# Kernel optimization log

Hardware: AMD Instinct MI355X
Metric: run time of the kernel (lower is better)

The kernel has to match this reference:

```python
import jax, jax.numpy as jnp
import numpy as np

N_NODES = 50000
N_EDGES = 600000
N_COMM = 500
COMM_EDGES = 8000
NFEAT = 128
NHID = 128
NCLASS = 10
NLAYERS = 3
NHEADS = 8
EPS = 1e-5


def setup_inputs() -> dict:
    key = jax.random.key(0)
    ks = jax.random.split(key, 32)
    s = 0.05
    def rn(i, shape, scale=s):
        return (jax.random.normal(ks[i], shape, dtype=jnp.float32) * scale)
    return {
        "node_features": jax.random.normal(ks[0], (N_NODES, NFEAT), dtype=jnp.float32),
        "node_edge_index": jax.random.randint(ks[1], (2, N_EDGES), 0, N_NODES),
        "comm_features": jax.random.normal(ks[2], (N_COMM, NHID), dtype=jnp.float32),
        "comm_edge_index": jax.random.randint(ks[3], (2, COMM_EDGES), 0, N_COMM),
        "node_to_comm_map": jax.random.randint(ks[4], (N_NODES,), 0, N_COMM),
        # node-branch GCN params (nfeat == nhid so weights stack)
        "node_W": rn(5, (NLAYERS, NHID, NHID)),
        "node_b": rn(6, (NLAYERS, NHID)),
        "node_bn_g": 1.0 + rn(7, (NLAYERS, NHID)),
        "node_bn_b": rn(8, (NLAYERS, NHID)),
        # community-branch GCN params
        "comm_W": rn(9, (NLAYERS, NHID, NHID)),
        "comm_b": rn(10, (NLAYERS, NHID)),
        "comm_bn_g": 1.0 + rn(11, (NLAYERS, NHID)),
        "comm_bn_b": rn(12, (NLAYERS, NHID)),
        # MultiheadAttention params (torch layout: y = x @ W.T + b)
        "attn_in_w": rn(13, (3 * NHID, NHID)),
        "attn_in_b": rn(14, (3 * NHID,)),
        "attn_out_w": rn(15, (NHID, NHID)),
        "attn_out_b": rn(16, (NHID,)),
        # gate LayerNorm
        "ln_g": 1.0 + rn(17, (NHID,)),
        "ln_b": rn(18, (NHID,)),
        # classifier: Linear(128,64) -> BN -> ReLU -> Linear(64,10)
        "cls_W1": rn(19, (NHID, NHID // 2)),
        "cls_b1": rn(20, (NHID // 2,)),
        "cls_bn_g": 1.0 + rn(21, (NHID // 2,)),
        "cls_bn_b": rn(22, (NHID // 2,)),
        "cls_W2": rn(23, (NHID // 2, NCLASS)),
        "cls_b2": rn(24, (NCLASS,)),
    }


def _gcn_norm(edge_index, n):
    # PyG gcn_norm: add self-loops, symmetric D^-1/2 (A+I) D^-1/2
    loop = jnp.arange(n)
    src = jnp.concatenate([edge_index[0], loop])
    dst = jnp.concatenate([edge_index[1], loop])
    deg = jax.ops.segment_sum(jnp.ones(src.shape[0], jnp.float32), dst, num_segments=n)
    dinv = jnp.where(deg > 0, deg ** -0.5, 0.0)
    return src, dst, dinv[src] * dinv[dst]


def _gcn_stack(x, edge_index, Ws, bs, gs, betas):
    n = x.shape[0]
    src, dst, norm = _gcn_norm(edge_index, n)
    h = x
    for i in range(Ws.shape[0]):
        h_prev = h
        m = h @ Ws[i]  # linear commutes with normalized aggregation
        agg = jax.ops.segment_sum(m[src] * norm[:, None], dst, num_segments=n) + bs[i]
        mu = agg.mean(0)
        var = agg.var(0)  # biased, as torch BN training
        hb = (agg - mu) / jnp.sqrt(var + EPS) * gs[i] + betas[i]
        h = jax.nn.relu(hb)
        if i > 0:
            h = h + h_prev
    return h


def _mha(x, wi, bi, wo, bo):
    # x: [N, S=2, E]
    N, S, E = x.shape
    dh = E // NHEADS
    qkv = x @ wi.T + bi
    q, k, v = jnp.split(qkv, 3, axis=-1)
    q = q.reshape(N, S, NHEADS, dh)
    k = k.reshape(N, S, NHEADS, dh)
    v = v.reshape(N, S, NHEADS, dh)
    att = jnp.einsum('nqhd,nkhd->nhqk', q, k) / np.float32(np.sqrt(dh))
    att = jax.nn.softmax(att, axis=-1)
    o = jnp.einsum('nhqk,nkhd->nqhd', att, v).reshape(N, S, E)
    return o @ wo.T + bo


def reference(node_features, node_edge_index, comm_features, comm_edge_index,
              node_to_comm_map, node_W, node_b, node_bn_g, node_bn_b,
              comm_W, comm_b, comm_bn_g, comm_bn_b,
              attn_in_w, attn_in_b, attn_out_w, attn_out_b,
              ln_g, ln_b, cls_W1, cls_b1, cls_bn_g, cls_bn_b, cls_W2, cls_b2):
    h_node = _gcn_stack(node_features, node_edge_index, node_W, node_b, node_bn_g, node_bn_b)
    h_comm = _gcn_stack(comm_features, comm_edge_index, comm_W, comm_b, comm_bn_g, comm_bn_b)
    safe = jnp.clip(node_to_comm_map, 0, h_comm.shape[0] - 1)
    h_comm_exp = h_comm[safe]  # [N, nhid] cross-scale gather
    comb = jnp.stack([h_node, h_comm_exp], axis=1)  # [N, 2, nhid]
    attended = _mha(comb, attn_in_w, attn_in_b, attn_out_w, attn_out_b)
    x = attended.mean(axis=1) + h_node
    mu = x.mean(-1, keepdims=True)
    var = x.var(-1, keepdims=True)
    h_final = (x - mu) / jnp.sqrt(var + EPS) * ln_g + ln_b
    z = h_final @ cls_W1 + cls_b1
    zm = z.mean(0)
    zv = z.var(0)
    z = jax.nn.relu((z - zm) / jnp.sqrt(zv + EPS) * cls_bn_g + cls_bn_b)
    logits = z @ cls_W2 + cls_b2
    return jax.nn.log_softmax(logits, axis=-1)
```

## Files before the change

### kernel.cpp

```cpp
#include <hip/hip_runtime.h>
#include <hip/hip_bf16.h>
#include <cstdint>
#include <cstddef>


typedef __attribute__((ext_vector_type(8))) short bf16x8;
typedef __attribute__((ext_vector_type(4))) float f32x4;

#define EPSV 1e-5f

__device__ __forceinline__ float b2f(unsigned short u) {
    union { unsigned int i; float f; } x; x.i = ((unsigned int)u) << 16; return x.f;
}
__device__ __forceinline__ unsigned short f2b(float f) {
    union { float f; unsigned int i; } x; x.f = f;
    unsigned int i = x.i;
    return (unsigned short)((i + 0x7fffu + ((i >> 16) & 1u)) >> 16);
}

__global__ void prep_kernel(const float* __restrict__ node_W, const float* __restrict__ comm_W,
                            const float* __restrict__ cls_W1, const float* __restrict__ attn_in_w,
                            const float* __restrict__ attn_out_w, const float* __restrict__ comm_feat,
                            const float* __restrict__ node_feat,
                            unsigned short* __restrict__ WtN, unsigned short* __restrict__ WtC,
                            unsigned short* __restrict__ W1t, unsigned short* __restrict__ WinB,
                            unsigned short* __restrict__ WoutB, unsigned short* __restrict__ cfb,
                            unsigned short* __restrict__ nfb, int nC128, int nN128,
                            uint4* __restrict__ nreg, int nn4,
                            const int* __restrict__ ndst, int* __restrict__ cnt_n, int nE,
                            const int* __restrict__ cdst, int* __restrict__ cnt_c, int cE) {
    int idx = blockIdx.x * 256 + threadIdx.x;
    if (idx < 49152) {
        int l = idx >> 14, e = idx & 16383;
        int j = e & 7, lane = (e >> 3) & 63, kc = (e >> 9) & 3, t = e >> 11;
        int col = t * 16 + (lane & 15);
        int k = (lane >> 4) * 8 + kc * 32 + j;
        WtN[idx] = f2b(node_W[l * 16384 + k * 128 + col]); return;
    }
    idx -= 49152;
    if (idx < 49152) {
        int l = idx >> 14, e = idx & 16383;
        int j = e & 7, lane = (e >> 3) & 63, kc = (e >> 9) & 3, t = e >> 11;
        int col = t * 16 + (lane & 15);
        int k = (lane >> 4) * 8 + kc * 32 + j;
        WtC[idx] = f2b(comm_W[l * 16384 + k * 128 + col]); return;
    }
    idx -= 49152;
    if (idx < 8192) {
        int e = idx;
        int j = e & 7, lane = (e >> 3) & 63, kc = (e >> 9) & 3, t = e >> 11;
        int col = t * 16 + (lane & 15);
        int k = (lane >> 4) * 8 + kc * 32 + j;
        W1t[idx] = f2b(cls_W1[k * 64 + col]); return;
    }
    idx -= 8192;
    if (idx < 49152) {
        int e = idx;
        int j = e & 7, lane = (e >> 3) & 63, kc = (e >> 9) & 3, t = e >> 11;
        int col = t * 16 + (lane & 15);
        int k = (lane >> 4) * 8 + kc * 32 + j;
        WinB[idx] = f2b(attn_in_w[col * 128 + k]); return;
    }
    idx -= 49152;
    if (idx < 16384) {
        int e = idx;
        int j = e & 7, lane = (e >> 3) & 63, kc = (e >> 9) & 3, t = e >> 11;
        int col = t * 16 + (lane & 15);
        int k = (lane >> 4) * 8 + kc * 32 + j;
        WoutB[idx] = f2b(attn_out_w[col * 128 + k]); return;
    }
    idx -= 16384;
    if (idx < nC128) { cfb[idx] = f2b(comm_feat[idx]); return; }
    idx -= nC128;
    if (idx < nN128) { nfb[idx] = f2b(node_feat[idx]); return; }
    idx -= nN128;
    if (idx < nn4) {
        uint4 v; v.x = 0xFFFFFFFFu; v.y = 0xFFFFFFFFu; v.z = 0xFFFFFFFFu; v.w = 0xFFFFFFFFu;
        nreg[idx] = v; return;
    }
    idx -= nn4;
    if (idx < nE) { atomicAdd(&cnt_n[ndst[idx]], 1); return; }
    idx -= nE;
    if (idx < cE) atomicAdd(&cnt_c[cdst[idx]], 1);
}

__global__ void scan_block_dual(const int* __restrict__ cnt_n, int* __restrict__ rs_n,
                                int* __restrict__ bsum_n, int nN, int nbN,
                                const int* __restrict__ cnt_c, int* __restrict__ rs_c,
                                int* __restrict__ bsum_c, int nC,
                                float* __restrict__ di_n, float* __restrict__ di_c) {
    __shared__ int tmp[2048];
    int nbC = (nC + 1023) >> 10;
    int extra = (int)blockIdx.x - (nbN + nbC);
    if (extra >= 0) {
        int g = extra * 1024 + (int)threadIdx.x;
        if (g < nN) di_n[g] = rsqrtf((float)cnt_n[g] + 1.0f);
        else { int gc = g - nN; if (gc < nC) di_c[gc] = rsqrtf((float)cnt_c[gc] + 1.0f); }
        return;
    }
    const int* cnt; int* excl; int* bsum; int n, lb;
    if ((int)blockIdx.x < nbN) { cnt = cnt_n; excl = rs_n; bsum = bsum_n; n = nN; lb = blockIdx.x; }
    else { cnt = cnt_c; excl = rs_c; bsum = bsum_c; n = nC; lb = blockIdx.x - nbN; }
    int tid = threadIdx.x;
    int gid = lb * 1024 + tid;
    int v = (gid < n) ? ((cnt[gid] + 7) & ~7) : 0;
    int buf = 0;
    tmp[tid] = v;
    __syncthreads();
    for (int d = 1; d < 1024; d <<= 1) {
        int t = tmp[buf * 1024 + tid];
        int add = (tid >= d) ? tmp[buf * 1024 + tid - d] : 0;
        tmp[(1 - buf) * 1024 + tid] = t + add;
        buf = 1 - buf;
        __syncthreads();
    }
    int inc = tmp[buf * 1024 + tid];
    if (gid < n) excl[gid] = inc - v;
    if (tid == 1023) bsum[lb] = inc;
}

__global__ void scan_add_dual(int* __restrict__ rs_n, const int* __restrict__ bsum_n,
                              int* __restrict__ cur_n, int nN,
                              int* __restrict__ rs_c, const int* __restrict__ bsum_c,
                              int* __restrict__ cur_c, int nC) {
    int gid = blockIdx.x * 256 + threadIdx.x;
    if (gid < nN) {
        int lb = gid >> 10;
        int p = 0;
        for (int i = 0; i < lb; ++i) p += bsum_n[i];
        int v = rs_n[gid] + p;
        rs_n[gid] = v; cur_n[gid] = v;
    } else {
        int g = gid - nN;
        if (g < nC) {
            int lb = g >> 10;
            int p = 0;
            for (int i = 0; i < lb; ++i) p += bsum_c[i];
            int v = rs_c[g] + p;
            rs_c[g] = v; cur_c[g] = v;
        }
    }
}

__device__ __forceinline__ void gemm_wave_128(const unsigned short* __restrict__ A,
                                              const unsigned short* __restrict__ Bt,
                                              const float* __restrict__ di,
                                              unsigned short* __restrict__ D,
                                              int M, int m0, int lane) {
    int r = lane & 15, q = lane >> 4;
    int arow = m0 + r; if (arow >= M) arow = M - 1;
    const unsigned short* ap = A + (size_t)arow * 128 + q * 8;
    bf16x8 afrag[4];
#pragma unroll
    for (int kc = 0; kc < 4; ++kc)
        afrag[kc] = *(const bf16x8*)(const void*)(ap + kc * 32);
    float dsc[4];
#pragma unroll
    for (int t = 0; t < 4; ++t) {
        int row = m0 + q * 4 + t; if (row >= M) row = M - 1;
        dsc[t] = di[row];
    }
#pragma unroll
    for (int tt = 0; tt < 8; ++tt) {
        f32x4 acc = {0.f, 0.f, 0.f, 0.f};
#pragma unroll
        for (int kc = 0; kc < 4; ++kc) {
            bf16x8 bfrag = *(const bf16x8*)(const void*)(Bt + (((size_t)tt * 4 + kc) << 9) + lane * 8);
            acc = __builtin_amdgcn_mfma_f32_16x16x32_bf16(afrag[kc], bfrag, acc, 0, 0, 0);
        }
        int n0 = tt * 16;
#pragma unroll
        for (int t = 0; t < 4; ++t) {
            int row = m0 + q * 4 + t;
            if (row < M) D[(size_t)row * 128 + n0 + r] = f2b(acc[t] * dsc[t]);
        }
    }
}

__global__ __launch_bounds__(256) void gemm_dual(
    const unsigned short* __restrict__ A0, const unsigned short* __restrict__ Bt0,
    const float* __restrict__ di0, unsigned short* __restrict__ D0, int M0, int blocksA,
    const unsigned short* __restrict__ A1, const unsigned short* __restrict__ Bt1,
    const float* __restrict__ di1, unsigned short* __restrict__ D1, int M1) {
    int blk = blockIdx.x;
    const unsigned short *A, *Bt; const float* di; unsigned short* D; int M, lb;
    if (blk < blocksA) { A = A0; Bt = Bt0; di = di0; D = D0; M = M0; lb = blk; }
    else { A = A1; Bt = Bt1; di = di1; D = D1; M = M1; lb = blk - blocksA; }
    int m0 = (lb * 4 + (int)(threadIdx.x >> 6)) * 16;
    if (m0 >= M) return;
    gemm_wave_128(A, Bt, di, D, M, m0, threadIdx.x & 63);
}

__global__ __launch_bounds__(256) void gemm_fill_kernel(
    const unsigned short* __restrict__ A0, const unsigned short* __restrict__ Bt0,
    const float* __restrict__ di0, unsigned short* __restrict__ D0, int M0, int blocksA,
    const unsigned short* __restrict__ A1, const unsigned short* __restrict__ Bt1,
    const float* __restrict__ di1, unsigned short* __restrict__ D1, int M1, int blocksB,
    const int* __restrict__ ns, const int* __restrict__ ndst,
    int* __restrict__ cur_n, unsigned short* __restrict__ csrc_n, int nE,
    const int* __restrict__ cs, const int* __restrict__ cdst,
    int* __restrict__ cur_c, unsigned short* __restrict__ csrc_c, int cE) {
    int blk = blockIdx.x;
    if (blk < blocksA + blocksB) {
        const unsigned short *A, *Bt; const float* di; unsigned short* D; int M, lb;
        if (blk < blocksA) { A = A0; Bt = Bt0; di = di0; D = D0; M = M0; lb = blk; }
        else { A = A1; Bt = Bt1; di = di1; D = D1; M = M1; lb = blk - blocksA; }
        int m0 = (lb * 4 + (int)(threadIdx.x >> 6)) * 16;
        if (m0 >= M) return;
        gemm_wave_128(A, Bt, di, D, M, m0, threadIdx.x & 63);
        return;
    }
    int e = (blk - blocksA - blocksB) * 256 + threadIdx.x;
    if (e < nE) {
        int s = ns[e], d = ndst[e];
        int pos = atomicAdd(&cur_n[d], 1);
        __builtin_nontemporal_store((unsigned short)s, csrc_n + pos);
    } else if (e - nE < cE) {
        int ee = e - nE;
        int s = cs[ee], d = cdst[ee];
        int pos = atomicAdd(&cur_c[d], 1);
        __builtin_nontemporal_store((unsigned short)s, csrc_c + pos);
    }
}

__global__ __launch_bounds__(256) void gather_dual(
    const unsigned short* __restrict__ m0, const int* __restrict__ rs0,
    const int* __restrict__ cnt0, const unsigned short* __restrict__ cs0,
    const float* __restrict__ di0, const float* __restrict__ b0,
    float* __restrict__ agg0, float* __restrict__ bins0, int n0, int blocksA,
    const unsigned short* __restrict__ m1, const int* __restrict__ rs1,
    const int* __restrict__ cnt1, const unsigned short* __restrict__ cs1,
    const float* __restrict__ di1, const float* __restrict__ b1,
    float* __restrict__ agg1, float* __restrict__ bins1, int n1) {
    __shared__ float lsum[4][128], lsq[4][128];
    int blk = blockIdx.x;
    const unsigned short* m; const int *rs, *cnt; const unsigned short* cs;
    const float *di, *bias;
    float *agg, *bins; int n, lb;
    if (blk < blocksA) { m = m0; rs = rs0; cnt = cnt0; cs = cs0; di = di0; bias = b0; agg = agg0; bins = bins0; n = n0; lb = blk; }
    else { m = m1; rs = rs1; cnt = cnt1; cs = cs1; di = di1; bias = b1; agg = agg1; bins = bins1; n = n1; lb = blk - blocksA; }
    int wib = threadIdx.x >> 6, lane = threadIdx.x & 63;
    int node = lb * 4 + wib;
    bool act = node < n;
    float a0 = 0.f, a1 = 0.f;
    if (act) {
        int start = rs[node];
        int end = start + ((cnt[node] + 7) & ~7);
        for (int i = start; i < end; i += 8) {
            int s[8]; unsigned int v[8];
#pragma unroll
            for (int j = 0; j < 8; ++j) s[j] = cs[i + j];
#pragma unroll
            for (int j = 0; j < 8; ++j) {
                int si = s[j] < n ? s[j] : node;
                v[j] = *(const unsigned int*)(m + (size_t)si * 128 + 2 * lane);
            }
#pragma unroll
            for (int j = 0; j < 8; ++j) {
                float wj = s[j] < n ? 1.f : 0.f;
                a0 += b2f((unsigned short)(v[j] & 0xffff)) * wj;
                a1 += b2f((unsigned short)(v[j] >> 16)) * wj;
            }
        }
        unsigned int v = *(const unsigned int*)(m + (size_t)node * 128 + 2 * lane);
        a0 += b2f((unsigned short)(v & 0xffff));
        a1 += b2f((unsigned short)(v >> 16));
        float d = di[node];
        a0 = a0 * d + bias[2 * lane];
        a1 = a1 * d + bias[2 * lane + 1];
        float2 o; o.x = a0; o.y = a1;
        ((float2*)(agg + (size_t)node * 128))[lane] = o;
    }
    lsum[wib][2 * lane] = a0;       lsum[wib][2 * lane + 1] = a1;
    lsq[wib][2 * lane] = a0 * a0;   lsq[wib][2 * lane + 1] = a1 * a1;
    __syncthreads();
    int t = threadIdx.x;
    int bb = (lb & 31) * 256;
    if (t < 128) {
        float v = lsum[0][t] + lsum[1][t] + lsum[2][t] + lsum[3][t];
        atomicAdd(&bins[bb + t], v);
    } else {
        int c = t - 128;
        float v = lsq[0][c] + lsq[1][c] + lsq[2][c] + lsq[3][c];
        atomicAdd(&bins[bb + 128 + c], v);
    }
}

__global__ __launch_bounds__(256) void apply_dual(
    const float* __restrict__ agg0, const float* __restrict__ bins0,
    const float* __restrict__ g0, const float* __restrict__ be0,
    unsigned short* __restrict__ hb0, int n0, int blocksA, int useRes,
    const float* __restrict__ agg1, const float* __restrict__ bins1,
    const float* __restrict__ g1, const float* __restrict__ be1,
    unsigned short* __restrict__ hb1, int n1,
    int doCq, const unsigned short* __restrict__ WinB,
    const float* __restrict__ binb, float* __restrict__ cqkv) {
    __shared__ float sc[128], sh[128], bs[256];
    __shared__ unsigned short crow_s[32 * 136];
    int blk = blockIdx.x;
    bool isComm = blk >= blocksA;
    const float *agg, *bins, *g, *be; unsigned short* hb; int n, lb;
    if (!isComm) { agg = agg0; bins = bins0; g = g0; be = be0; hb = hb0; n = n0; lb = blk; }
    else { agg = agg1; bins = bins1; g = g1; be = be1; hb = hb1; n = n1; lb = blk - blocksA; }
    int t = threadIdx.x;
    {
        float a = 0.f;
#pragma unroll
        for (int b = 0; b < 32; ++b) a += bins[b * 256 + t];
        bs[t] = a;
    }
    __syncthreads();
    if (t < 128) {
        float inv = 1.f / (float)n;
        float mean = bs[t] * inv;
        float var = bs[128 + t] * inv - mean * mean;
        float rstd = rsqrtf(var + EPSV);
        float s = g[t] * rstd;
        sc[t] = s;
        sh[t] = be[t] - mean * s;
    }
    __syncthreads();
    bool stage = doCq && isComm;
#pragma unroll
    for (int it = 0; it < 4; ++it) {
        int base = (lb * 4 + it) * 1024 + t * 4;
        if (base < n * 128) {
            float4 a = *(const float4*)(agg + base);
            ushort4 h = *(const ushort4*)(hb + base);
            int f = base & 127;
            float v0 = fmaxf(a.x * sc[f] + sh[f], 0.f);
            float v1 = fmaxf(a.y * sc[f + 1] + sh[f + 1], 0.f);
            float v2 = fmaxf(a.z * sc[f + 2] + sh[f + 2], 0.f);
            float v3 = fmaxf(a.w * sc[f + 3] + sh[f + 3], 0.f);
            if (useRes) { v0 += b2f(h.x); v1 += b2f(h.y); v2 += b2f(h.z); v3 += b2f(h.w); }
            ushort4 o; o.x = f2b(v0); o.y = f2b(v1); o.z = f2b(v2); o.w = f2b(v3);
            *(ushort4*)(hb + base) = o;
            if (stage) {
                int row = (base >> 7) - lb * 32;
                *(ushort4*)(crow_s + row * 136 + (base & 127)) = o;
            }
        }
    }
    if (stage) {
        __syncthreads();
        int lane = t & 63, w = t >> 6;
        int r = lane & 15, q = lane >> 4;
        int rg = w & 1;
        const unsigned short* ap = crow_s + (rg * 16 + r) * 136 + q * 8;
        bf16x8 afrag[4];
#pragma unroll
        for (int kc = 0; kc < 4; ++kc)
            afrag[kc] = *(const bf16x8*)(const void*)(ap + kc * 32);
        int t0 = (w >> 1) * 12;
        for (int tt = t0; tt < t0 + 12; ++tt) {
            f32x4 acc = {0.f, 0.f, 0.f, 0.f};
#pragma unroll
            for (int kc = 0; kc < 4; ++kc) {
                bf16x8 bfrag = *(const bf16x8*)(const void*)(WinB + (((size_t)tt * 4 + kc) << 9) + lane * 8);
                acc = __builtin_amdgcn_mfma_f32_16x16x32_bf16(afrag[kc], bfrag, acc, 0, 0, 0);
            }
            int n0c = tt * 16;
            float bv = binb[n0c + r];
#pragma unroll
            for (int t4 = 0; t4 < 4; ++t4) {
                int row = lb * 32 + rg * 16 + q * 4 + t4;
                if (row < n) cqkv[(size_t)row * 384 + n0c + r] = acc[t4] + bv;
            }
        }
    }
}

__global__ __launch_bounds__(256) void mha_fused_kernel(
    const unsigned short* __restrict__ hbn, const int* __restrict__ map,
    const float* __restrict__ cqkv,
    const unsigned short* __restrict__ WinB, const float* __restrict__ bin,
    const unsigned short* __restrict__ WoutB, const float* __restrict__ bout,
    const float* __restrict__ lng, const float* __restrict__ lnb,
    const unsigned short* __restrict__ W1t, const float* __restrict__ b1v,
    float* __restrict__ z, float* __restrict__ zbins, int nN, int nC) {
    __shared__ unsigned short obf_s[16 * 144];
    __shared__ float att_s[16 * 132];

    int b = blockIdx.x;
    int hg = threadIdx.x >> 6;
    int lane = threadIdx.x & 63;
    int r = lane & 15, q = lane >> 4;

    int arow = b * 16 + r; if (arow >= nN) arow = nN - 1;
    const unsigned short* ap = hbn + (size_t)arow * 128 + q * 8;
    bf16x8 afrag[4];
#pragma unroll
    for (int kc = 0; kc < 4; ++kc)
        afrag[kc] = *(const bf16x8*)(const void*)(ap + kc * 32);

    const float* cp[4];
#pragma unroll
    for (int t = 0; t < 4; ++t) {
        int nt = b * 16 + q * 4 + t; if (nt >= nN) nt = nN - 1;
        int c = map[nt]; c = c < 0 ? 0 : (c >= nC ? nC - 1 : c);
        cp[t] = cqkv + (size_t)c * 384;
    }

#pragma unroll
    for (int c = 0; c < 2; ++c) {
        int h = hg * 2 + c;
        f32x4 qa, ka, va;
#pragma unroll
        for (int p = 0; p < 3; ++p) {
            int tt = p * 8 + h;
            f32x4 acc = {0.f, 0.f, 0.f, 0.f};
#pragma unroll
            for (int kc = 0; kc < 4; ++kc) {
                bf16x8 bfrag = *(const bf16x8*)(const void*)(WinB + (((size_t)tt * 4 + kc) << 9) + lane * 8);
                acc = __builtin_amdgcn_mfma_f32_16x16x32_bf16(afrag[kc], bfrag, acc, 0, 0, 0);
            }
            float bv = bin[tt * 16 + r];
#pragma unroll
            for (int t = 0; t < 4; ++t) acc[t] += bv;
            if (p == 0) qa = acc; else if (p == 1) ka = acc; else va = acc;
        }
        float qc[4], kc_[4], vc[4];
#pragma unroll
        for (int t = 0; t < 4; ++t) {
            const float* cpt = cp[t] + h * 16 + r;
            qc[t] = cpt[0]; kc_[t] = cpt[128]; vc[t] = cpt[256];
        }
#pragma unroll
        for (int t = 0; t < 4; ++t) {
            float s00 = qa[t] * ka[t];
            float s01 = qa[t] * kc_[t];
            float s10 = qc[t] * ka[t];
            float s11 = qc[t] * kc_[t];
#pragma unroll
            for (int mku = 1; mku <= 8; mku <<= 1) {
                s00 += __shfl_xor(s00, mku); s01 += __shfl_xor(s01, mku);
                s10 += __shfl_xor(s10, mku); s11 += __shfl_xor(s11, mku);
            }
            s00 *= 0.25f; s01 *= 0.25f; s10 *= 0.25f; s11 *= 0.25f;
            float m0 = fmaxf(s00, s01), m1 = fmaxf(s10, s11);
            float e00 = __expf(s00 - m0), e01 = __expf(s01 - m0);
            float e10 = __expf(s10 - m1), e11 = __expf(s11 - m1);
            float i0 = 1.f / (e00 + e01), i1 = 1.f / (e10 + e11);
            float o0 = (e00 * va[t] + e01 * vc[t]) * i0;
            float o1 = (e10 * va[t] + e11 * vc[t]) * i1;
            obf_s[(q * 4 + t) * 144 + h * 16 + r] = f2b(0.5f * (o0 + o1));
        }
    }
    __syncthreads();

    bf16x8 ofrag[4];
#pragma unroll
    for (int kc = 0; kc < 4; ++kc)
        ofrag[kc] = *(const bf16x8*)(const void*)(obf_s + r * 144 + q * 8 + kc * 32);
#pragma unroll
    for (int c = 0; c < 2; ++c) {
        int tt = hg * 2 + c;
        f32x4 acc = {0.f, 0.f, 0.f, 0.f};
#pragma unroll
        for (int kc = 0; kc < 4; ++kc) {
            bf16x8 bfrag = *(const bf16x8*)(const void*)(WoutB + (((size_t)tt * 4 + kc) << 9) + lane * 8);
            acc = __builtin_amdgcn_mfma_f32_16x16x32_bf16(ofrag[kc], bfrag, acc, 0, 0, 0);
        }
        int n0 = tt * 16;
        float bv = bout[n0 + r];
#pragma unroll
        for (int t = 0; t < 4; ++t)
            att_s[(q * 4 + t) * 132 + n0 + r] = acc[t] + bv;
    }
    __syncthreads();
    unsigned short* hf_s = obf_s;

    {
        int nl = threadIdx.x >> 4;
        int j = threadIdx.x & 15;
        int gnode = b * 16 + nl;
        if (gnode >= nN) gnode = nN - 1;
        const unsigned short* hrow = hbn + (size_t)gnode * 128 + j * 8;
        ushort4 ha = *(const ushort4*)(hrow);
        ushort4 hbv = *(const ushort4*)(hrow + 4);
        float x[8]; float s = 0.f, s2 = 0.f;
        x[0] = att_s[nl * 132 + j * 8 + 0] + b2f(ha.x);
        x[1] = att_s[nl * 132 + j * 8 + 1] + b2f(ha.y);
        x[2] = att_s[nl * 132 + j * 8 + 2] + b2f(ha.z);
        x[3] = att_s[nl * 132 + j * 8 + 3] + b2f(ha.w);
        x[4] = att_s[nl * 132 + j * 8 + 4] + b2f(hbv.x);
        x[5] = att_s[nl * 132 + j * 8 + 5] + b2f(hbv.y);
        x[6] = att_s[nl * 132 + j * 8 + 6] + b2f(hbv.z);
        x[7] = att_s[nl * 132 + j * 8 + 7] + b2f(hbv.w);
#pragma unroll
        for (int i = 0; i < 8; ++i) { s += x[i]; s2 += x[i] * x[i]; }
        s += __shfl_xor(s, 1);  s2 += __shfl_xor(s2, 1);
        s += __shfl_xor(s, 2);  s2 += __shfl_xor(s2, 2);
        s += __shfl_xor(s, 4);  s2 += __shfl_xor(s2, 4);
        s += __shfl_xor(s, 8);  s2 += __shfl_xor(s2, 8);
        float mu = s * (1.f / 128.f);
        float var = s2 * (1.f / 128.f) - mu * mu;
        float rstd = rsqrtf(var + EPSV);
        ushort4 o1, o2;
        o1.x = f2b((x[0] - mu) * rstd * lng[j * 8 + 0] + lnb[j * 8 + 0]);
        o1.y = f2b((x[1] - mu) * rstd * lng[j * 8 + 1] + lnb[j * 8 + 1]);
        o1.z = f2b((x[2] - mu) * rstd * lng[j * 8 + 2] + lnb[j * 8 + 2]);
        o1.w = f2b((x[3] - mu) * rstd * lng[j * 8 + 3] + lnb[j * 8 + 3]);
        o2.x = f2b((x[4] - mu) * rstd * lng[j * 8 + 4] + lnb[j * 8 + 4]);
        o2.y = f2b((x[5] - mu) * rstd * lng[j * 8 + 5] + lnb[j * 8 + 5]);
        o2.z = f2b((x[6] - mu) * rstd * lng[j * 8 + 6] + lnb[j * 8 + 6]);
        o2.w = f2b((x[7] - mu) * rstd * lng[j * 8 + 7] + lnb[j * 8 + 7]);
        *(ushort4*)(hf_s + nl * 136 + j * 8) = o1;
        *(ushort4*)(hf_s + nl * 136 + j * 8 + 4) = o2;
    }
    __syncthreads();

    {
        bf16x8 hfrag[4];
#pragma unroll
        for (int kc = 0; kc < 4; ++kc)
            hfrag[kc] = *(const bf16x8*)(const void*)(hf_s + r * 136 + q * 8 + kc * 32);
        f32x4 acc = {0.f, 0.f, 0.f, 0.f};
#pragma unroll
        for (int kc = 0; kc < 4; ++kc) {
            bf16x8 bfrag = *(const bf16x8*)(const void*)(W1t + (((size_t)hg * 4 + kc) << 9) + lane * 8);
            acc = __builtin_amdgcn_mfma_f32_16x16x32_bf16(hfrag[kc], bfrag, acc, 0, 0, 0);
        }
        float bv = b1v[hg * 16 + r];
        float s = 0.f, s2 = 0.f;
#pragma unroll
        for (int t = 0; t < 4; ++t) {
            int row = b * 16 + q * 4 + t;
            if (row < nN) {
                float v = acc[t] + bv;
                z[(size_t)row * 64 + hg * 16 + r] = v;
                s += v; s2 += v * v;
            }
        }
        s += __shfl_xor(s, 16);  s2 += __shfl_xor(s2, 16);
        s += __shfl_xor(s, 32);  s2 += __shfl_xor(s2, 32);
        if (lane < 16) {
            int bb = (b & 31) * 128;
            atomicAdd(&zbins[bb + hg * 16 + r], s);
            atomicAdd(&zbins[bb + 64 + hg * 16 + r], s2);
        }
    }
}

__global__ __launch_bounds__(256) void final_kernel(const float* __restrict__ z,
                                                    const float* __restrict__ zbins,
                                                    const float* __restrict__ g,
                                                    const float* __restrict__ be,
                                                    const float* __restrict__ W2,
                                                    const float* __restrict__ b2v,
                                                    float* __restrict__ out, int nN) {
    __shared__ float zs[128];
    int t = threadIdx.x;
    if (t < 128) {
        float a = 0.f;
#pragma unroll
        for (int b = 0; b < 32; ++b) a += zbins[b * 128 + t];
        zs[t] = a;
    }
    __syncthreads();
    int lane = t & 63;
    float inv = 1.f / (float)nN;
    float mean = zs[lane] * inv;
    float var = zs[64 + lane] * inv - mean * mean;
    float sc = g[lane] * rsqrtf(var + EPSV);
    float sh = be[lane] - mean * sc;
    const float* wrow = W2 + lane * 10;
#pragma unroll
    for (int it = 0; it < 4; ++it) {
        int node = blockIdx.x * 16 + (t >> 6) * 4 + it;
        float v = 0.f;
        if (node < nN) v = fmaxf(z[(size_t)node * 64 + lane] * sc + sh, 0.f);
        float p[10];
#pragma unroll
        for (int c = 0; c < 10; ++c) p[c] = v * wrow[c];
#pragma unroll
        for (int off = 32; off >= 1; off >>= 1) {
#pragma unroll
            for (int c = 0; c < 10; ++c) p[c] += __shfl_xor(p[c], off);
        }
        if (node < nN) {
            float l[10], mx = -1e30f;
#pragma unroll
            for (int c = 0; c < 10; ++c) { l[c] = p[c] + b2v[c]; mx = fmaxf(mx, l[c]); }
            float se = 0.f;
#pragma unroll
            for (int c = 0; c < 10; ++c) se += expf(l[c] - mx);
            float lse = mx + logf(se);
            if (lane < 10) out[(size_t)node * 10 + lane] = l[lane] - lse;
        }
    }
}

static inline int cdiv(long a, long b) { return (int)((a + b - 1) / b); }

extern "C" void kernel_launch(void* const* d_in, const int* in_sizes, int n_in,
                              void* d_out, int out_size, void* d_ws, size_t ws_size,
                              hipStream_t stream) {
    const float* node_feat = (const float*)d_in[0];
    const int*   nedge     = (const int*)d_in[1];
    const float* comm_feat = (const float*)d_in[2];
    const int*   cedge     = (const int*)d_in[3];
    const int*   n2c       = (const int*)d_in[4];
    const float* node_W    = (const float*)d_in[5];
    const float* node_b    = (const float*)d_in[6];
    const float* node_g    = (const float*)d_in[7];
    const float* node_beta = (const float*)d_in[8];
    const float* comm_W    = (const float*)d_in[9];
    const float* comm_b    = (const float*)d_in[10];
    const float* comm_g    = (const float*)d_in[11];
    const float* comm_beta = (const float*)d_in[12];
    const float* attn_in_w = (const float*)d_in[13];
    const float* attn_in_b = (const float*)d_in[14];
    const float* attn_out_w= (const float*)d_in[15];
    const float* attn_out_b= (const float*)d_in[16];
    const float* ln_g      = (const float*)d_in[17];
    const float* ln_b      = (const float*)d_in[18];
    const float* cls_W1    = (const float*)d_in[19];
    const float* cls_b1    = (const float*)d_in[20];
    const float* cls_bn_g  = (const float*)d_in[21];
    const float* cls_bn_b  = (const float*)d_in[22];
    const float* cls_W2    = (const float*)d_in[23];
    const float* cls_b2    = (const float*)d_in[24];

    const int nN = in_sizes[0] / 128;
    const int nE = in_sizes[1] / 2;
    const int nC = in_sizes[2] / 128;
    const int cE = in_sizes[3] / 2;
    const int padE_n = nE + 8 * nN;
    const int padE_c = cE + 8 * nC;

    char* ws = (char*)d_ws;
    size_t off = 0;
    auto alloc = [&](size_t bytes) -> char* {
        char* p = ws + off;
        off = (off + bytes + 255) & ~(size_t)255;
        return p;
    };
    size_t zero_begin = off;
    int*   cnt_n  = (int*)alloc((size_t)nN * 4);
    int*   cur_n  = (int*)alloc((size_t)nN * 4);
    int*   cnt_c  = (int*)alloc((size_t)nC * 4);
    int*   cur_c  = (int*)alloc((size_t)nC * 4);
    float* bins_n = (float*)alloc((size_t)3 * 32 * 256 * 4);
    float* bins_c = (float*)alloc((size_t)3 * 32 * 256 * 4);
    float* zbins  = (float*)alloc((size_t)32 * 128 * 4);
    size_t zero_bytes = off - zero_begin;
    size_t neg_begin = off;
    unsigned short* csrc_n = (unsigned short*)alloc((size_t)padE_n * 2);
    unsigned short* csrc_c = (unsigned short*)alloc((size_t)padE_c * 2);
    size_t neg_bytes = off - neg_begin;
    int*   rs_n   = (int*)alloc((size_t)(nN + 1) * 4);
    int*   bsum_n = (int*)alloc(256 * 4);
    float* dinv_n = (float*)alloc((size_t)nN * 4);
    int*   rs_c   = (int*)alloc((size_t)(nC + 1) * 4);
    int*   bsum_c = (int*)alloc(256 * 4);
    float* dinv_c = (float*)alloc((size_t)nC * 4);
    unsigned short* hb_n  = (unsigned short*)alloc((size_t)nN * 256);
    unsigned short* hb_c  = (unsigned short*)alloc((size_t)nC * 256);
    unsigned short* cfb   = (unsigned short*)alloc((size_t)nC * 256);
    unsigned short* m_cb  = (unsigned short*)alloc((size_t)nC * 256);
    float*          agg_c = (float*)alloc((size_t)nC * 512);
    float*          cqkv  = (float*)alloc((size_t)nC * 384 * 4);
    unsigned short* WtN  = (unsigned short*)alloc((size_t)3 * 16384 * 2);
    unsigned short* WtC  = (unsigned short*)alloc((size_t)3 * 16384 * 2);
    unsigned short* W1t  = (unsigned short*)alloc((size_t)64 * 128 * 2);
    unsigned short* WinB = (unsigned short*)alloc((size_t)384 * 128 * 2);
    unsigned short* WoutB= (unsigned short*)alloc((size_t)128 * 128 * 2);
    unsigned short* m_nb = (unsigned short*)alloc((size_t)nN * 256);
    float*          agg_n= (float*)alloc((size_t)nN * 512);
    unsigned short* nfb  = (unsigned short*)agg_n;
    float*          z    = agg_n;

    hipMemsetAsync(ws + zero_begin, 0, zero_bytes, stream);

    int nn4 = (int)(neg_bytes / 16);
    long prepN = 49152L * 3 + 8192 + 16384 + (long)nC * 128 + (long)nN * 128;
    long prepTotal = prepN + nn4 + nE + cE;
    prep_kernel<<<cdiv(prepTotal, 256), 256, 0, stream>>>(
        node_W, comm_W, cls_W1, attn_in_w, attn_out_w, comm_feat, node_feat,
        WtN, WtC, W1t, WinB, WoutB, cfb, nfb, nC * 128, nN * 128,
        (uint4*)(ws + neg_begin), nn4,
        nedge + nE, cnt_n, nE, cedge + cE, cnt_c, cE);

    int nbN = cdiv(nN, 1024), nbC = cdiv(nC, 1024);
    int dinvB = cdiv((long)nN + nC, 1024);
    scan_block_dual<<<nbN + nbC + dinvB, 1024, 0, stream>>>(
        cnt_n, rs_n, bsum_n, nN, nbN, cnt_c, rs_c, bsum_c, nC, dinv_n, dinv_c);
    scan_add_dual<<<cdiv((long)nN + nC, 256), 256, 0, stream>>>(
        rs_n, bsum_n, cur_n, nN, rs_c, bsum_c, cur_c, nC);

    int gemmA = cdiv(nN, 64), gemmB = cdiv(nC, 64);
    int fillB = cdiv((long)nE + cE, 256);
    int gatA = cdiv(nN, 4), gatB = cdiv(nC, 4);
    int appA = cdiv((long)nN * 128, 4096), appB = cdiv((long)nC * 128, 4096);
    for (int i = 0; i < 3; ++i) {
        float* bn_i = bins_n + (size_t)i * 32 * 256;
        float* bc_i = bins_c + (size_t)i * 32 * 256;
        if (i == 0) {
            gemm_fill_kernel<<<gemmA + gemmB + fillB, 256, 0, stream>>>(
                nfb, WtN, dinv_n, m_nb, nN, gemmA,
                cfb, WtC, dinv_c, m_cb, nC, gemmB,
                nedge, nedge + nE, cur_n, csrc_n, nE,
                cedge, cedge + cE, cur_c, csrc_c, cE);
        } else {
            gemm_dual<<<gemmA + gemmB, 256, 0, stream>>>(
                hb_n, WtN + i * 16384, dinv_n, m_nb, nN, gemmA,
                hb_c, WtC + i * 16384, dinv_c, m_cb, nC);
        }
        gather_dual<<<gatA + gatB, 256, 0, stream>>>(
            m_nb, rs_n, cnt_n, csrc_n, dinv_n, node_b + i * 128, agg_n, bn_i, nN, gatA,
            m_cb, rs_c, cnt_c, csrc_c, dinv_c, comm_b + i * 128, agg_c, bc_i, nC);
        apply_dual<<<appA + appB, 256, 0, stream>>>(
            agg_n, bn_i, node_g + i * 128, node_beta + i * 128, hb_n, nN, appA, i > 0 ? 1 : 0,
            agg_c, bc_i, comm_g + i * 128, comm_beta + i * 128, hb_c, nC,
            i == 2 ? 1 : 0, WinB, attn_in_b, cqkv);
    }

    mha_fused_kernel<<<cdiv(nN, 16), 256, 0, stream>>>(
        hb_n, n2c, cqkv, WinB, attn_in_b, WoutB, attn_out_b, ln_g, ln_b,
        W1t, cls_b1, z, zbins, nN, nC);

    final_kernel<<<cdiv(nN, 16), 256, 0, stream>>>(
        z, zbins, cls_bn_g, cls_bn_b, cls_W2, cls_b2, (float*)d_out, nN);
}
```

Measured before the change: 449.9 us.

## Fuse BN-apply with next-layer GEMM and encode CSR sources with zero sentinel

```diff
diff --git a/kernel.cpp b/kernel.cpp
--- a/kernel.cpp
+++ b/kernel.cpp
@@ -26,7 +26,6 @@
                             unsigned short* __restrict__ W1t, unsigned short* __restrict__ WinB,
                             unsigned short* __restrict__ WoutB, unsigned short* __restrict__ cfb,
                             unsigned short* __restrict__ nfb, int nC128, int nN128,
-                            uint4* __restrict__ nreg, int nn4,
                             const int* __restrict__ ndst, int* __restrict__ cnt_n, int nE,
                             const int* __restrict__ cdst, int* __restrict__ cnt_c, int cE) {
     int idx = blockIdx.x * 256 + threadIdx.x;
@@ -74,11 +73,6 @@
     idx -= nC128;
     if (idx < nN128) { nfb[idx] = f2b(node_feat[idx]); return; }
     idx -= nN128;
-    if (idx < nn4) {
-        uint4 v; v.x = 0xFFFFFFFFu; v.y = 0xFFFFFFFFu; v.z = 0xFFFFFFFFu; v.w = 0xFFFFFFFFu;
-        nreg[idx] = v; return;
-    }
-    idx -= nn4;
     if (idx < nE) { atomicAdd(&cnt_n[ndst[idx]], 1); return; }
     idx -= nE;
     if (idx < cE) atomicAdd(&cnt_c[cdst[idx]], 1);
@@ -177,29 +171,15 @@
     }
 }
 
-__global__ __launch_bounds__(256) void gemm_dual(
-    const unsigned short* __restrict__ A0, const unsigned short* __restrict__ Bt0,
-    const float* __restrict__ di0, unsigned short* __restrict__ D0, int M0, int blocksA,
-    const unsigned short* __restrict__ A1, const unsigned short* __restrict__ Bt1,
-    const float* __restrict__ di1, unsigned short* __restrict__ D1, int M1) {
-    int blk = blockIdx.x;
-    const unsigned short *A, *Bt; const float* di; unsigned short* D; int M, lb;
-    if (blk < blocksA) { A = A0; Bt = Bt0; di = di0; D = D0; M = M0; lb = blk; }
-    else { A = A1; Bt = Bt1; di = di1; D = D1; M = M1; lb = blk - blocksA; }
-    int m0 = (lb * 4 + (int)(threadIdx.x >> 6)) * 16;
-    if (m0 >= M) return;
-    gemm_wave_128(A, Bt, di, D, M, m0, threadIdx.x & 63);
-}
-
 __global__ __launch_bounds__(256) void gemm_fill_kernel(
     const unsigned short* __restrict__ A0, const unsigned short* __restrict__ Bt0,
     const float* __restrict__ di0, unsigned short* __restrict__ D0, int M0, int blocksA,
     const unsigned short* __restrict__ A1, const unsigned short* __restrict__ Bt1,
     const float* __restrict__ di1, unsigned short* __restrict__ D1, int M1, int blocksB,
     const int* __restrict__ ns, const int* __restrict__ ndst,
-    int* __restrict__ cur_n, unsigned short* __restrict__ csrc_n, int nE,
+    int* __restrict__ cur_n, unsigned int* __restrict__ csrc_n, int nE,
     const int* __restrict__ cs, const int* __restrict__ cdst,
-    int* __restrict__ cur_c, unsigned short* __restrict__ csrc_c, int cE) {
+    int* __restrict__ cur_c, unsigned int* __restrict__ csrc_c, int cE) {
     int blk = blockIdx.x;
     if (blk < blocksA + blocksB) {
         const unsigned short *A, *Bt; const float* di; unsigned short* D; int M, lb;
@@ -214,12 +194,12 @@
     if (e < nE) {
         int s = ns[e], d = ndst[e];
         int pos = atomicAdd(&cur_n[d], 1);
-        __builtin_nontemporal_store((unsigned short)s, csrc_n + pos);
+        atomicOr(&csrc_n[pos >> 1], (unsigned int)(s + 1) << ((pos & 1) * 16));
     } else if (e - nE < cE) {
         int ee = e - nE;
         int s = cs[ee], d = cdst[ee];
         int pos = atomicAdd(&cur_c[d], 1);
-        __builtin_nontemporal_store((unsigned short)s, csrc_c + pos);
+        atomicOr(&csrc_c[pos >> 1], (unsigned int)(s + 1) << ((pos & 1) * 16));
     }
 }
 
@@ -252,12 +232,12 @@
             for (int j = 0; j < 8; ++j) s[j] = cs[i + j];
 #pragma unroll
             for (int j = 0; j < 8; ++j) {
-                int si = s[j] < n ? s[j] : node;
+                int si = s[j] ? s[j] - 1 : node;
                 v[j] = *(const unsigned int*)(m + (size_t)si * 128 + 2 * lane);
             }
 #pragma unroll
             for (int j = 0; j < 8; ++j) {
-                float wj = s[j] < n ? 1.f : 0.f;
+                float wj = s[j] ? 1.f : 0.f;
                 a0 += b2f((unsigned short)(v[j] & 0xffff)) * wj;
                 a1 += b2f((unsigned short)(v[j] >> 16)) * wj;
             }
@@ -283,6 +263,94 @@
         int c = t - 128;
         float v = lsq[0][c] + lsq[1][c] + lsq[2][c] + lsq[3][c];
         atomicAdd(&bins[bb + 128 + c], v);
+    }
+}
+
+__global__ __launch_bounds__(256) void applygemm_dual(
+    const float* __restrict__ agg0, const float* __restrict__ bins0,
+    const float* __restrict__ g0, const float* __restrict__ be0,
+    unsigned short* __restrict__ hb0, const unsigned short* __restrict__ Bt0,
+    const float* __restrict__ di0, unsigned short* __restrict__ D0,
+    int n0, int blocksA, int useRes,
+    const float* __restrict__ agg1, const float* __restrict__ bins1,
+    const float* __restrict__ g1, const float* __restrict__ be1,
+    unsigned short* __restrict__ hb1, const unsigned short* __restrict__ Bt1,
+    const float* __restrict__ di1, unsigned short* __restrict__ D1, int n1) {
+    __shared__ float sc[128], sh[128], bs[256];
+    __shared__ unsigned short hrow_s[64 * 136];
+    int blk = blockIdx.x;
+    const float *agg, *bins, *g, *be, *di; unsigned short *hb, *D;
+    const unsigned short* Bt; int n, lb;
+    if (blk < blocksA) { agg = agg0; bins = bins0; g = g0; be = be0; hb = hb0; Bt = Bt0; di = di0; D = D0; n = n0; lb = blk; }
+    else { agg = agg1; bins = bins1; g = g1; be = be1; hb = hb1; Bt = Bt1; di = di1; D = D1; n = n1; lb = blk - blocksA; }
+    int t = threadIdx.x;
+    {
+        float a = 0.f;
+#pragma unroll
+        for (int b = 0; b < 32; ++b) a += bins[b * 256 + t];
+        bs[t] = a;
+    }
+    __syncthreads();
+    if (t < 128) {
+        float inv = 1.f / (float)n;
+        float mean = bs[t] * inv;
+        float var = bs[128 + t] * inv - mean * mean;
+        float rstd = rsqrtf(var + EPSV);
+        float s = g[t] * rstd;
+        sc[t] = s;
+        sh[t] = be[t] - mean * s;
+    }
+    __syncthreads();
+    int row0 = lb * 64;
+#pragma unroll
+    for (int it = 0; it < 8; ++it) {
+        int base = row0 * 128 + it * 1024 + t * 4;
+        if (base < n * 128) {
+            float4 a = *(const float4*)(agg + base);
+            ushort4 h = *(const ushort4*)(hb + base);
+            int f = base & 127;
+            float v0 = fmaxf(a.x * sc[f] + sh[f], 0.f);
+            float v1 = fmaxf(a.y * sc[f + 1] + sh[f + 1], 0.f);
+            float v2 = fmaxf(a.z * sc[f + 2] + sh[f + 2], 0.f);
+            float v3 = fmaxf(a.w * sc[f + 3] + sh[f + 3], 0.f);
+            if (useRes) { v0 += b2f(h.x); v1 += b2f(h.y); v2 += b2f(h.z); v3 += b2f(h.w); }
+            ushort4 o; o.x = f2b(v0); o.y = f2b(v1); o.z = f2b(v2); o.w = f2b(v3);
+            *(ushort4*)(hb + base) = o;
+            int lr = (base >> 7) - row0;
+            *(ushort4*)(hrow_s + lr * 136 + f) = o;
+        }
+    }
+    __syncthreads();
+    int lane = t & 63, w = t >> 6;
+    int m0 = row0 + w * 16;
+    if (m0 >= n) return;
+    int r = lane & 15, q = lane >> 4;
+    int arow = m0 + r; if (arow >= n) arow = n - 1;
+    const unsigned short* ap = hrow_s + (arow - row0) * 136 + q * 8;
+    bf16x8 afrag[4];
+#pragma unroll
+    for (int kc = 0; kc < 4; ++kc)
+        afrag[kc] = *(const bf16x8*)(const void*)(ap + kc * 32);
+    float dsc[4];
+#pragma unroll
+    for (int t4 = 0; t4 < 4; ++t4) {
+        int row = m0 + q * 4 + t4; if (row >= n) row = n - 1;
+        dsc[t4] = di[row];
+    }
+#pragma unroll
+    for (int tt = 0; tt < 8; ++tt) {
+        f32x4 acc = {0.f, 0.f, 0.f, 0.f};
+#pragma unroll
+        for (int kc = 0; kc < 4; ++kc) {
+            bf16x8 bfrag = *(const bf16x8*)(const void*)(Bt + (((size_t)tt * 4 + kc) << 9) + lane * 8);
+            acc = __builtin_amdgcn_mfma_f32_16x16x32_bf16(afrag[kc], bfrag, acc, 0, 0, 0);
+        }
+        int n0c = tt * 16;
+#pragma unroll
+        for (int t4 = 0; t4 < 4; ++t4) {
+            int row = m0 + q * 4 + t4;
+            if (row < n) D[(size_t)row * 128 + n0c + r] = f2b(acc[t4] * dsc[t4]);
+        }
     }
 }
 
@@ -644,11 +712,9 @@
     float* bins_n = (float*)alloc((size_t)3 * 32 * 256 * 4);
     float* bins_c = (float*)alloc((size_t)3 * 32 * 256 * 4);
     float* zbins  = (float*)alloc((size_t)32 * 128 * 4);
+    unsigned int* csrc_n = (unsigned int*)alloc((size_t)((padE_n + 1) / 2) * 4);
+    unsigned int* csrc_c = (unsigned int*)alloc((size_t)((padE_c + 1) / 2) * 4);
     size_t zero_bytes = off - zero_begin;
-    size_t neg_begin = off;
-    unsigned short* csrc_n = (unsigned short*)alloc((size_t)padE_n * 2);
-    unsigned short* csrc_c = (unsigned short*)alloc((size_t)padE_c * 2);
-    size_t neg_bytes = off - neg_begin;
     int*   rs_n   = (int*)alloc((size_t)(nN + 1) * 4);
     int*   bsum_n = (int*)alloc(256 * 4);
     float* dinv_n = (float*)alloc((size_t)nN * 4);
@@ -673,13 +739,11 @@
 
     hipMemsetAsync(ws + zero_begin, 0, zero_bytes, stream);
 
-    int nn4 = (int)(neg_bytes / 16);
     long prepN = 49152L * 3 + 8192 + 16384 + (long)nC * 128 + (long)nN * 128;
-    long prepTotal = prepN + nn4 + nE + cE;
+    long prepTotal = prepN + nE + cE;
     prep_kernel<<<cdiv(prepTotal, 256), 256, 0, stream>>>(
         node_W, comm_W, cls_W1, attn_in_w, attn_out_w, comm_feat, node_feat,
         WtN, WtC, W1t, WinB, WoutB, cfb, nfb, nC * 128, nN * 128,
-        (uint4*)(ws + neg_begin), nn4,
         nedge + nE, cnt_n, nE, cedge + cE, cnt_c, cE);
 
     int nbN = cdiv(nN, 1024), nbC = cdiv(nC, 1024);
@@ -693,28 +757,31 @@
     int fillB = cdiv((long)nE + cE, 256);
     int gatA = cdiv(nN, 4), gatB = cdiv(nC, 4);
     int appA = cdiv((long)nN * 128, 4096), appB = cdiv((long)nC * 128, 4096);
-    for (int i = 0; i < 3; ++i) {
-        float* bn_i = bins_n + (size_t)i * 32 * 256;
-        float* bc_i = bins_c + (size_t)i * 32 * 256;
-        if (i == 0) {
-            gemm_fill_kernel<<<gemmA + gemmB + fillB, 256, 0, stream>>>(
-                nfb, WtN, dinv_n, m_nb, nN, gemmA,
-                cfb, WtC, dinv_c, m_cb, nC, gemmB,
-                nedge, nedge + nE, cur_n, csrc_n, nE,
-                cedge, cedge + cE, cur_c, csrc_c, cE);
-        } else {
-            gemm_dual<<<gemmA + gemmB, 256, 0, stream>>>(
-                hb_n, WtN + i * 16384, dinv_n, m_nb, nN, gemmA,
-                hb_c, WtC + i * 16384, dinv_c, m_cb, nC);
-        }
-        gather_dual<<<gatA + gatB, 256, 0, stream>>>(
-            m_nb, rs_n, cnt_n, csrc_n, dinv_n, node_b + i * 128, agg_n, bn_i, nN, gatA,
-            m_cb, rs_c, cnt_c, csrc_c, dinv_c, comm_b + i * 128, agg_c, bc_i, nC);
-        apply_dual<<<appA + appB, 256, 0, stream>>>(
-            agg_n, bn_i, node_g + i * 128, node_beta + i * 128, hb_n, nN, appA, i > 0 ? 1 : 0,
-            agg_c, bc_i, comm_g + i * 128, comm_beta + i * 128, hb_c, nC,
-            i == 2 ? 1 : 0, WinB, attn_in_b, cqkv);
-    }
+
+    gemm_fill_kernel<<<gemmA + gemmB + fillB, 256, 0, stream>>>(
+        nfb, WtN, dinv_n, m_nb, nN, gemmA,
+        cfb, WtC, dinv_c, m_cb, nC, gemmB,
+        nedge, nedge + nE, cur_n, csrc_n, nE,
+        cedge, cedge + cE, cur_c, csrc_c, cE);
+    gather_dual<<<gatA + gatB, 256, 0, stream>>>(
+        m_nb, rs_n, cnt_n, (const unsigned short*)csrc_n, dinv_n, node_b, agg_n, bins_n, nN, gatA,
+        m_cb, rs_c, cnt_c, (const unsigned short*)csrc_c, dinv_c, comm_b, agg_c, bins_c, nC);
+    applygemm_dual<<<gemmA + gemmB, 256, 0, stream>>>(
+        agg_n, bins_n, node_g, node_beta, hb_n, WtN + 16384, dinv_n, m_nb, nN, gemmA, 0,
+        agg_c, bins_c, comm_g, comm_beta, hb_c, WtC + 16384, dinv_c, m_cb, nC);
+    gather_dual<<<gatA + gatB, 256, 0, stream>>>(
+        m_nb, rs_n, cnt_n, (const unsigned short*)csrc_n, dinv_n, node_b + 128, agg_n, bins_n + 32 * 256, nN, gatA,
+        m_cb, rs_c, cnt_c, (const unsigned short*)csrc_c, dinv_c, comm_b + 128, agg_c, bins_c + 32 * 256, nC);
+    applygemm_dual<<<gemmA + gemmB, 256, 0, stream>>>(
+        agg_n, bins_n + 32 * 256, node_g + 128, node_beta + 128, hb_n, WtN + 2 * 16384, dinv_n, m_nb, nN, gemmA, 1,
+        agg_c, bins_c + 32 * 256, comm_g + 128, comm_beta + 128, hb_c, WtC + 2 * 16384, dinv_c, m_cb, nC);
+    gather_dual<<<gatA + gatB, 256, 0, stream>>>(
+        m_nb, rs_n, cnt_n, (const unsigned short*)csrc_n, dinv_n, node_b + 256, agg_n, bins_n + 2 * 32 * 256, nN, gatA,
+        m_cb, rs_c, cnt_c, (const unsigned short*)csrc_c, dinv_c, comm_b + 256, agg_c, bins_c + 2 * 32 * 256, nC);
+    apply_dual<<<appA + appB, 256, 0, stream>>>(
+        agg_n, bins_n + 2 * 32 * 256, node_g + 256, node_beta + 256, hb_n, nN, appA, 1,
+        agg_c, bins_c + 2 * 32 * 256, comm_g + 256, comm_beta + 256, hb_c, nC,
+        1, WinB, attn_in_b, cqkv);
 
     mha_fused_kernel<<<cdiv(nN, 16), 256, 0, stream>>>(
         hb_n, n2c, cqkv, WinB, attn_in_b, WoutB, attn_out_b, ln_g, ln_b,
```

Measured after the change: 449.4 us. No clear change (-0.1%).
